# Kernel tuning notes

Measured on AMD Instinct MI355X. Metric: run time of the kernel, lower is better.

Reference implementation:

```python
import jax, jax.numpy as jnp
import numpy as np

WH, WW = 8, 8
N = WH * WW
DIM = 128
H = 4
B_ = 8192


def _make_buffers():
    # relative_coords_table: [1, 2Wh-1, 2Ww-1, 2]
    ch = np.arange(-(WH - 1), WH, dtype=np.float32)
    cw = np.arange(-(WW - 1), WW, dtype=np.float32)
    gh, gw = np.meshgrid(ch, cw, indexing='ij')
    table = np.stack([gh, gw], axis=-1)[None]  # [1, 2Wh-1, 2Ww-1, 2]
    table[..., 0] /= (WH - 1 + 1e-12)
    table[..., 1] /= (WW - 1 + 1e-12)
    table *= 8.0
    table = np.sign(table) * np.log2(np.abs(table) + 1.0) / np.log2(8.0)
    # relative_position_index: [N, N]
    yh, yw = np.meshgrid(np.arange(WH), np.arange(WW), indexing='ij')
    coords = np.stack([yh, yw]).reshape(2, -1)  # [2, N]
    rel = coords[:, :, None] - coords[:, None, :]  # [2, N, N]
    rel = rel.transpose(1, 2, 0).astype(np.int64)
    rel[..., 0] += WH - 1
    rel[..., 1] += WW - 1
    rel[..., 0] *= 2 * WW - 1
    idx = rel.sum(-1)
    return jnp.asarray(table, jnp.float32), jnp.asarray(idx, jnp.int32)


def setup_inputs() -> dict:
    key = jax.random.key(0)
    ks = jax.random.split(key, 9)
    s = 0.02
    rel_table, rel_index = _make_buffers()
    return {
        'x': jax.random.normal(ks[0], (B_, N, DIM), jnp.float32),
        'W_qkv': jax.random.normal(ks[1], (3 * DIM, DIM), jnp.float32) * s,
        'q_bias': jax.random.normal(ks[2], (DIM,), jnp.float32) * s,
        'v_bias': jax.random.normal(ks[3], (DIM,), jnp.float32) * s,
        'logit_scale': jnp.full((H, 1, 1), jnp.log(10.0), jnp.float32),
        'cpb_w1': jax.random.normal(ks[4], (512, 2), jnp.float32) * s,
        'cpb_b1': jax.random.normal(ks[5], (512,), jnp.float32) * s,
        'cpb_w2': jax.random.normal(ks[6], (H, 512), jnp.float32) * s,
        'proj_w': jax.random.normal(ks[7], (DIM, DIM), jnp.float32) * s,
        'proj_b': jax.random.normal(ks[8], (DIM,), jnp.float32) * s,
        'rel_table': rel_table,
        'rel_index': rel_index,
    }


def reference(x, W_qkv, q_bias, v_bias, logit_scale, cpb_w1, cpb_b1, cpb_w2,
              proj_w, proj_b, rel_table, rel_index):
    B, n, C = x.shape
    hd = C // H
    # qkv projection with Swin-V2 bias layout (k bias frozen at zero)
    qkv_bias = jnp.concatenate([q_bias, jnp.zeros_like(v_bias), v_bias])
    qkv = x @ W_qkv.T + qkv_bias               # [B, N, 3C]
    qkv = qkv.reshape(B, n, 3, H, hd).transpose(2, 0, 3, 1, 4)
    q, k, v = qkv[0], qkv[1], qkv[2]           # [B, H, N, hd]
    # cosine attention
    qn = q / jnp.maximum(jnp.linalg.norm(q, axis=-1, keepdims=True), 1e-12)
    kn = k / jnp.maximum(jnp.linalg.norm(k, axis=-1, keepdims=True), 1e-12)
    attn = jnp.einsum('bhnd,bhmd->bhnm', qn, kn)
    scale = jnp.exp(jnp.minimum(logit_scale, jnp.log(1.0 / 0.01)))  # [H,1,1]
    attn = attn * scale
    # continuous position bias MLP -> gather -> 16*sigmoid
    hmid = jax.nn.relu(rel_table @ cpb_w1.T + cpb_b1)      # [1,15,15,512]
    bias_table = (hmid @ cpb_w2.T).reshape(-1, H)          # [(2Wh-1)(2Ww-1), H]
    rpb = bias_table[rel_index.reshape(-1)].reshape(n, n, H)
    rpb = 16.0 * jax.nn.sigmoid(rpb.transpose(2, 0, 1))    # [H, N, N]
    attn = jax.nn.softmax(attn + rpb[None], axis=-1)
    out = jnp.einsum('bhnm,bhmd->bhnd', attn, v)           # [B, H, N, hd]
    out = out.transpose(0, 2, 1, 3).reshape(B, n, C)
    return out @ proj_w.T + proj_b
```

## Files before the change

kernel.cpp:

```cpp
#include <hip/hip_runtime.h>

typedef short bf16x8 __attribute__((ext_vector_type(8)));
typedef float f32x4 __attribute__((ext_vector_type(4)));

__device__ __forceinline__ unsigned cvt_pk_bf16(float lo, float hi) {
  unsigned r;
  asm("v_cvt_pk_bf16_f32 %0, %1, %2" : "=v"(r) : "v"(lo), "v"(hi));
  return r;
}

__device__ __forceinline__ bf16x8 pack4(unsigned a, unsigned b, unsigned c, unsigned d) {
  union { unsigned u[4]; bf16x8 v; } t;
  t.u[0] = a; t.u[1] = b; t.u[2] = c; t.u[3] = d;
  return t.v;
}

__device__ __forceinline__ unsigned short f2bf(float f) {
  unsigned u = __float_as_uint(f);
  unsigned r = (u + 0x7fffu + ((u >> 16) & 1u)) >> 16;
  return (unsigned short)r;
}

__global__ __launch_bounds__(256) void prep(
    const float* __restrict__ W_qkv, const float* __restrict__ proj_w,
    const float* __restrict__ cpb_w1, const float* __restrict__ cpb_b1,
    const float* __restrict__ cpb_w2, const float* __restrict__ rel_table,
    const int* __restrict__ rel_index,
    bf16x8* __restrict__ wq, bf16x8* __restrict__ wp, float* __restrict__ rpbf)
{
  const int b = blockIdx.x, t = threadIdx.x;
  if (b < 32) {
    int g = b * 256 + t;
    if (g < 6144) {
      int c = g >> 8, kk = (g >> 6) & 3, l = g & 63;
      const float* s = W_qkv + (c * 16 + (l & 15)) * 128 + kk * 32 + (l >> 4) * 8;
      bf16x8 v;
      #pragma unroll
      for (int j = 0; j < 8; ++j) v[j] = (short)f2bf(s[j]);
      wq[g] = v;
    } else {
      int gl = g - 6144;
      int c = gl >> 8, kk = (gl >> 6) & 3, l = gl & 63;
      const float* row = proj_w + (c * 16 + (l & 15)) * 128;
      bf16x8 v;
      #pragma unroll
      for (int j = 0; j < 8; ++j)
        v[j] = (short)f2bf(row[kk * 32 + (j >> 2) * 16 + (l >> 4) * 4 + (j & 3)]);
      wp[gl] = v;
    }
  } else {
    __shared__ float bt[900];
    if (t < 225) {
      float t0 = rel_table[t * 2], t1 = rel_table[t * 2 + 1];
      float a0 = 0.f, a1 = 0.f, a2 = 0.f, a3 = 0.f;
      for (int j = 0; j < 512; ++j) {
        float hm = fmaxf(t0 * cpb_w1[j * 2] + t1 * cpb_w1[j * 2 + 1] + cpb_b1[j], 0.f);
        a0 += hm * cpb_w2[j];
        a1 += hm * cpb_w2[512 + j];
        a2 += hm * cpb_w2[1024 + j];
        a3 += hm * cpb_w2[1536 + j];
      }
      bt[t * 4 + 0] = a0; bt[t * 4 + 1] = a1;
      bt[t * 4 + 2] = a2; bt[t * 4 + 3] = a3;
    }
    __syncthreads();
    for (int i = t; i < 16384; i += 256) {
      int hrc = i >> 8, lane = (i >> 2) & 63, j = i & 3;
      int hh = hrc >> 4, r = (hrc >> 2) & 3, c = hrc & 3;
      int n = r * 16 + (lane & 15);
      int m = c * 16 + ((lane >> 4) << 2) + j;
      float v = bt[rel_index[n * 64 + m] * 4 + hh];
      rpbf[i] = 16.0f * __fdividef(1.0f, 1.0f + __expf(-v));
    }
  }
}

__global__ __launch_bounds__(256, 3) void win_attn(
    const float* __restrict__ x,
    const float* __restrict__ q_bias,
    const float* __restrict__ v_bias,
    const float* __restrict__ logit_scale,
    const float* __restrict__ proj_b,
    const float* __restrict__ rpbf,
    const bf16x8* __restrict__ wq,
    const bf16x8* __restrict__ wp,
    float* __restrict__ out)
{
  __shared__ __align__(128) char lds[16384];
  const int tid  = threadIdx.x;
  const int lane = tid & 63;
  const int h    = tid >> 6;
  const int l15  = lane & 15;
  const int l4   = lane >> 4;
  const int swl  = (l15 & 7) << 4;
  const long base = (long)blockIdx.x * 8192;
  const f32x4 fzero = {0.f, 0.f, 0.f, 0.f};

  {
    const float4* xp = (const float4*)(x + base);
    #pragma unroll
    for (int i = 0; i < 8; ++i) {
      float4 v = xp[i * 256 + tid];
      int e   = (i * 256 + tid) * 4;
      int row = e >> 7;
      int cb  = (e & 127) * 2;
      uint2 pk = { cvt_pk_bf16(v.x, v.y), cvt_pk_bf16(v.z, v.w) };
      *(uint2*)(lds + ((row * 256 + cb) ^ ((row & 7) << 4))) = pk;
    }
  }
  __syncthreads();

  bf16x8 aq[4], bk[4], bv[2][2];

  {
    f32x4 qT[2][4], kT[2][4];
    #pragma unroll
    for (int ct = 0; ct < 2; ++ct)
      #pragma unroll
      for (int rt = 0; rt < 4; ++rt) { qT[ct][rt] = fzero; kT[ct][rt] = fzero; }

    #pragma unroll
    for (int kk = 0; kk < 4; ++kk) {
      bf16x8 a[4];
      #pragma unroll
      for (int rt = 0; rt < 4; ++rt) {
        int row = rt * 16 + l15;
        a[rt] = *(const bf16x8*)(lds + ((row * 256 + kk * 64 + l4 * 16) ^ swl));
      }
      #pragma unroll
      for (int ct = 0; ct < 2; ++ct) {
        bf16x8 wqf = wq[((2 * h + ct) * 4 + kk) * 64 + lane];
        bf16x8 wkf = wq[((8 + 2 * h + ct) * 4 + kk) * 64 + lane];
        #pragma unroll
        for (int rt = 0; rt < 4; ++rt) {
          qT[ct][rt] = __builtin_amdgcn_mfma_f32_16x16x32_bf16(wqf, a[rt], qT[ct][rt], 0, 0, 0);
          kT[ct][rt] = __builtin_amdgcn_mfma_f32_16x16x32_bf16(wkf, a[rt], kT[ct][rt], 0, 0, 0);
        }
      }
    }

    float scale = __expf(fminf(logit_scale[h], 4.6051701859880914f));
    float4 qb0 = *(const float4*)&q_bias[h * 32 + l4 * 4];
    float4 qb1 = *(const float4*)&q_bias[h * 32 + 16 + l4 * 4];
    #pragma unroll
    for (int rt = 0; rt < 4; ++rt) {
      float tq0 = qT[0][rt][0] + qb0.x, tq1 = qT[0][rt][1] + qb0.y;
      float tq2 = qT[0][rt][2] + qb0.z, tq3 = qT[0][rt][3] + qb0.w;
      float tq4 = qT[1][rt][0] + qb1.x, tq5 = qT[1][rt][1] + qb1.y;
      float tq6 = qT[1][rt][2] + qb1.z, tq7 = qT[1][rt][3] + qb1.w;
      float sq = tq0*tq0 + tq1*tq1 + tq2*tq2 + tq3*tq3
               + tq4*tq4 + tq5*tq5 + tq6*tq6 + tq7*tq7;
      float sk = kT[0][rt][0]*kT[0][rt][0] + kT[0][rt][1]*kT[0][rt][1]
               + kT[0][rt][2]*kT[0][rt][2] + kT[0][rt][3]*kT[0][rt][3]
               + kT[1][rt][0]*kT[1][rt][0] + kT[1][rt][1]*kT[1][rt][1]
               + kT[1][rt][2]*kT[1][rt][2] + kT[1][rt][3]*kT[1][rt][3];
      sq += __shfl_xor(sq, 16); sq += __shfl_xor(sq, 32);
      sk += __shfl_xor(sk, 16); sk += __shfl_xor(sk, 32);
      float iq = __fdividef(scale, fmaxf(sqrtf(sq), 1e-12f));
      float ik = __fdividef(1.0f,  fmaxf(sqrtf(sk), 1e-12f));
      aq[rt] = pack4(cvt_pk_bf16(tq0 * iq, tq1 * iq), cvt_pk_bf16(tq2 * iq, tq3 * iq),
                     cvt_pk_bf16(tq4 * iq, tq5 * iq), cvt_pk_bf16(tq6 * iq, tq7 * iq));
      bk[rt] = pack4(cvt_pk_bf16(kT[0][rt][0] * ik, kT[0][rt][1] * ik),
                     cvt_pk_bf16(kT[0][rt][2] * ik, kT[0][rt][3] * ik),
                     cvt_pk_bf16(kT[1][rt][0] * ik, kT[1][rt][1] * ik),
                     cvt_pk_bf16(kT[1][rt][2] * ik, kT[1][rt][3] * ik));
    }
  }

  {
    f32x4 vN[2][4];
    #pragma unroll
    for (int ct = 0; ct < 2; ++ct)
      #pragma unroll
      for (int rt = 0; rt < 4; ++rt) vN[ct][rt] = fzero;

    #pragma unroll
    for (int kk = 0; kk < 4; ++kk) {
      bf16x8 a[4];
      #pragma unroll
      for (int rt = 0; rt < 4; ++rt) {
        int row = rt * 16 + l15;
        a[rt] = *(const bf16x8*)(lds + ((row * 256 + kk * 64 + l4 * 16) ^ swl));
      }
      #pragma unroll
      for (int ct = 0; ct < 2; ++ct) {
        bf16x8 wvf = wq[((16 + 2 * h + ct) * 4 + kk) * 64 + lane];
        #pragma unroll
        for (int rt = 0; rt < 4; ++rt)
          vN[ct][rt] = __builtin_amdgcn_mfma_f32_16x16x32_bf16(a[rt], wvf, vN[ct][rt], 0, 0, 0);
      }
    }
    __syncthreads();

    float vb0 = v_bias[h * 32 + l15], vb1 = v_bias[h * 32 + 16 + l15];
    #pragma unroll
    for (int ks = 0; ks < 2; ++ks)
      #pragma unroll
      for (int ct = 0; ct < 2; ++ct) {
        float vb = ct ? vb1 : vb0;
        bv[ks][ct] = pack4(
            cvt_pk_bf16(vN[ct][2 * ks][0] + vb, vN[ct][2 * ks][1] + vb),
            cvt_pk_bf16(vN[ct][2 * ks][2] + vb, vN[ct][2 * ks][3] + vb),
            cvt_pk_bf16(vN[ct][2 * ks + 1][0] + vb, vN[ct][2 * ks + 1][1] + vb),
            cvt_pk_bf16(vN[ct][2 * ks + 1][2] + vb, vN[ct][2 * ks + 1][3] + vb));
      }
  }

  {
    const f32x4* rp = (const f32x4*)rpbf;
    #pragma unroll
    for (int r = 0; r < 4; ++r) {
      f32x4 st[4];
      #pragma unroll
      for (int c = 0; c < 4; ++c)
        st[c] = __builtin_amdgcn_mfma_f32_16x16x32_bf16(
            bk[c], aq[r], rp[(h * 16 + r * 4 + c) * 64 + lane], 0, 0, 0);

      float mx = st[0][0];
      #pragma unroll
      for (int c = 0; c < 4; ++c)
        #pragma unroll
        for (int j = 0; j < 4; ++j) mx = fmaxf(mx, st[c][j]);
      mx = fmaxf(mx, __shfl_xor(mx, 16));
      mx = fmaxf(mx, __shfl_xor(mx, 32));

      float e[4][4];
      float sum = 0.f;
      #pragma unroll
      for (int c = 0; c < 4; ++c)
        #pragma unroll
        for (int j = 0; j < 4; ++j) { e[c][j] = __expf(st[c][j] - mx); sum += e[c][j]; }
      sum += __shfl_xor(sum, 16); sum += __shfl_xor(sum, 32);
      float rs = __fdividef(1.0f, sum);

      bf16x8 ap0 = pack4(cvt_pk_bf16(e[0][0], e[0][1]), cvt_pk_bf16(e[0][2], e[0][3]),
                         cvt_pk_bf16(e[1][0], e[1][1]), cvt_pk_bf16(e[1][2], e[1][3]));
      bf16x8 ap1 = pack4(cvt_pk_bf16(e[2][0], e[2][1]), cvt_pk_bf16(e[2][2], e[2][3]),
                         cvt_pk_bf16(e[3][0], e[3][1]), cvt_pk_bf16(e[3][2], e[3][3]));

      f32x4 o0 = __builtin_amdgcn_mfma_f32_16x16x32_bf16(bv[0][0], ap0, fzero, 0, 0, 0);
      o0 = __builtin_amdgcn_mfma_f32_16x16x32_bf16(bv[1][0], ap1, o0, 0, 0, 0);
      f32x4 o1 = __builtin_amdgcn_mfma_f32_16x16x32_bf16(bv[0][1], ap0, fzero, 0, 0, 0);
      o1 = __builtin_amdgcn_mfma_f32_16x16x32_bf16(bv[1][1], ap1, o1, 0, 0, 0);

      int n = r * 16 + l15;
      uint4 w = { cvt_pk_bf16(o0[0] * rs, o0[1] * rs), cvt_pk_bf16(o0[2] * rs, o0[3] * rs),
                  cvt_pk_bf16(o1[0] * rs, o1[1] * rs), cvt_pk_bf16(o1[2] * rs, o1[3] * rs) };
      *(uint4*)(lds + ((n * 256 + h * 64 + 16 * l4) ^ ((n & 7) << 4))) = w;
    }
  }
  __syncthreads();

  {
    const int n = h * 16 + l15;
    f32x4 po[8];
    #pragma unroll
    for (int c2 = 0; c2 < 8; ++c2) po[c2] = fzero;
    #pragma unroll
    for (int kk = 0; kk < 4; ++kk) {
      bf16x8 ob = *(const bf16x8*)(lds + ((n * 256 + kk * 64 + 16 * l4) ^ swl));
      #pragma unroll
      for (int c2 = 0; c2 < 8; ++c2) {
        bf16x8 wf = wp[(c2 * 4 + kk) * 64 + lane];
        po[c2] = __builtin_amdgcn_mfma_f32_16x16x32_bf16(wf, ob, po[c2], 0, 0, 0);
      }
    }
    float* op = out + base + (long)n * 128;
    #pragma unroll
    for (int c2 = 0; c2 < 8; ++c2) {
      float4 pb = *(const float4*)&proj_b[c2 * 16 + l4 * 4];
      f32x4 v = { po[c2][0] + pb.x, po[c2][1] + pb.y,
                  po[c2][2] + pb.z, po[c2][3] + pb.w };
      __builtin_nontemporal_store(v, (f32x4*)&op[c2 * 16 + l4 * 4]);
    }
  }
}

extern "C" void kernel_launch(void* const* d_in, const int* in_sizes, int n_in,
                              void* d_out, int out_size, void* d_ws, size_t ws_size,
                              hipStream_t stream) {
  (void)n_in; (void)out_size; (void)ws_size;
  const float* x           = (const float*)d_in[0];
  const float* W_qkv       = (const float*)d_in[1];
  const float* q_bias      = (const float*)d_in[2];
  const float* v_bias      = (const float*)d_in[3];
  const float* logit_scale = (const float*)d_in[4];
  const float* cpb_w1      = (const float*)d_in[5];
  const float* cpb_b1      = (const float*)d_in[6];
  const float* cpb_w2      = (const float*)d_in[7];
  const float* proj_w      = (const float*)d_in[8];
  const float* proj_b      = (const float*)d_in[9];
  const float* rel_table   = (const float*)d_in[10];
  const int*   rel_index   = (const int*)d_in[11];

  float*  rpbf = (float*)d_ws;
  bf16x8* wq   = (bf16x8*)((char*)d_ws + 65536);
  bf16x8* wp   = (bf16x8*)((char*)d_ws + 65536 + 98304);

  int nwin = in_sizes[0] / 8192;

  prep<<<33, 256, 0, stream>>>(W_qkv, proj_w, cpb_w1, cpb_b1, cpb_w2,
                               rel_table, rel_index, wq, wp, rpbf);
  win_attn<<<nwin, 256, 0, stream>>>(x, q_bias, v_bias, logit_scale, proj_b,
                                     rpbf, wq, wp, (float*)d_out);
}
```

Before: 221.1 us.

## Use exp2 softmax with prescaled logits, add MFMA priority hints, repartition projection

Folds log2(e) into the cosine-attention scale and the position-bias table (16*log2e), so the softmax can use exp2f directly. Wraps MFMA blocks in s_setprio raises so matrix work is favoured over other waves. Changes the output projection so each wave computes all 64 rows for its own two 16-column tiles instead of 16 rows by all 128 columns. The weight fragments loaded per wave drop to a quarter, at the cost of four LDS reads per kk step, and the non-temporal stores become ordinary stores.

New measurement: 250.9 us. 13.5% more time.

```diff
diff --git a/kernel.cpp b/kernel.cpp
--- a/kernel.cpp
+++ b/kernel.cpp
@@ -70,7 +70,7 @@
       int n = r * 16 + (lane & 15);
       int m = c * 16 + ((lane >> 4) << 2) + j;
       float v = bt[rel_index[n * 64 + m] * 4 + hh];
-      rpbf[i] = 16.0f * __fdividef(1.0f, 1.0f + __expf(-v));
+      rpbf[i] = 23.083120654223414f * __fdividef(1.0f, 1.0f + __expf(-v));
     }
   }
 }
@@ -131,15 +131,18 @@
       for (int ct = 0; ct < 2; ++ct) {
         bf16x8 wqf = wq[((2 * h + ct) * 4 + kk) * 64 + lane];
         bf16x8 wkf = wq[((8 + 2 * h + ct) * 4 + kk) * 64 + lane];
+        __builtin_amdgcn_s_setprio(1);
         #pragma unroll
         for (int rt = 0; rt < 4; ++rt) {
           qT[ct][rt] = __builtin_amdgcn_mfma_f32_16x16x32_bf16(wqf, a[rt], qT[ct][rt], 0, 0, 0);
           kT[ct][rt] = __builtin_amdgcn_mfma_f32_16x16x32_bf16(wkf, a[rt], kT[ct][rt], 0, 0, 0);
         }
-      }
-    }
-
-    float scale = __expf(fminf(logit_scale[h], 4.6051701859880914f));
+        __builtin_amdgcn_s_setprio(0);
+      }
+    }
+
+    float scale = __expf(fminf(logit_scale[h], 4.6051701859880914f))
+                * 1.4426950408889634f;
     float4 qb0 = *(const float4*)&q_bias[h * 32 + l4 * 4];
     float4 qb1 = *(const float4*)&q_bias[h * 32 + 16 + l4 * 4];
     #pragma unroll
@@ -185,9 +188,11 @@
       #pragma unroll
       for (int ct = 0; ct < 2; ++ct) {
         bf16x8 wvf = wq[((16 + 2 * h + ct) * 4 + kk) * 64 + lane];
+        __builtin_amdgcn_s_setprio(1);
         #pragma unroll
         for (int rt = 0; rt < 4; ++rt)
           vN[ct][rt] = __builtin_amdgcn_mfma_f32_16x16x32_bf16(a[rt], wvf, vN[ct][rt], 0, 0, 0);
+        __builtin_amdgcn_s_setprio(0);
       }
     }
     __syncthreads();
@@ -211,10 +216,12 @@
     #pragma unroll
     for (int r = 0; r < 4; ++r) {
       f32x4 st[4];
+      __builtin_amdgcn_s_setprio(1);
       #pragma unroll
       for (int c = 0; c < 4; ++c)
         st[c] = __builtin_amdgcn_mfma_f32_16x16x32_bf16(
             bk[c], aq[r], rp[(h * 16 + r * 4 + c) * 64 + lane], 0, 0, 0);
+      __builtin_amdgcn_s_setprio(0);
 
       float mx = st[0][0];
       #pragma unroll
@@ -229,7 +236,7 @@
       #pragma unroll
       for (int c = 0; c < 4; ++c)
         #pragma unroll
-        for (int j = 0; j < 4; ++j) { e[c][j] = __expf(st[c][j] - mx); sum += e[c][j]; }
+        for (int j = 0; j < 4; ++j) { e[c][j] = exp2f(st[c][j] - mx); sum += e[c][j]; }
       sum += __shfl_xor(sum, 16); sum += __shfl_xor(sum, 32);
       float rs = __fdividef(1.0f, sum);
 
@@ -238,10 +245,12 @@
       bf16x8 ap1 = pack4(cvt_pk_bf16(e[2][0], e[2][1]), cvt_pk_bf16(e[2][2], e[2][3]),
                          cvt_pk_bf16(e[3][0], e[3][1]), cvt_pk_bf16(e[3][2], e[3][3]));
 
+      __builtin_amdgcn_s_setprio(1);
       f32x4 o0 = __builtin_amdgcn_mfma_f32_16x16x32_bf16(bv[0][0], ap0, fzero, 0, 0, 0);
       o0 = __builtin_amdgcn_mfma_f32_16x16x32_bf16(bv[1][0], ap1, o0, 0, 0, 0);
       f32x4 o1 = __builtin_amdgcn_mfma_f32_16x16x32_bf16(bv[0][1], ap0, fzero, 0, 0, 0);
       o1 = __builtin_amdgcn_mfma_f32_16x16x32_bf16(bv[1][1], ap1, o1, 0, 0, 0);
+      __builtin_amdgcn_s_setprio(0);
 
       int n = r * 16 + l15;
       uint4 w = { cvt_pk_bf16(o0[0] * rs, o0[1] * rs), cvt_pk_bf16(o0[2] * rs, o0[3] * rs),
@@ -252,26 +261,42 @@
   __syncthreads();
 
   {
-    const int n = h * 16 + l15;
-    f32x4 po[8];
-    #pragma unroll
-    for (int c2 = 0; c2 < 8; ++c2) po[c2] = fzero;
+    f32x4 po[4][2];
+    #pragma unroll
+    for (int rt = 0; rt < 4; ++rt)
+      #pragma unroll
+      for (int ci = 0; ci < 2; ++ci) po[rt][ci] = fzero;
+
     #pragma unroll
     for (int kk = 0; kk < 4; ++kk) {
-      bf16x8 ob = *(const bf16x8*)(lds + ((n * 256 + kk * 64 + 16 * l4) ^ swl));
-      #pragma unroll
-      for (int c2 = 0; c2 < 8; ++c2) {
-        bf16x8 wf = wp[(c2 * 4 + kk) * 64 + lane];
-        po[c2] = __builtin_amdgcn_mfma_f32_16x16x32_bf16(wf, ob, po[c2], 0, 0, 0);
-      }
-    }
-    float* op = out + base + (long)n * 128;
-    #pragma unroll
-    for (int c2 = 0; c2 < 8; ++c2) {
+      bf16x8 ob[4];
+      #pragma unroll
+      for (int rt = 0; rt < 4; ++rt) {
+        int row = rt * 16 + l15;
+        ob[rt] = *(const bf16x8*)(lds + ((row * 256 + kk * 64 + 16 * l4) ^ swl));
+      }
+      #pragma unroll
+      for (int ci = 0; ci < 2; ++ci) {
+        bf16x8 wf = wp[((2 * h + ci) * 4 + kk) * 64 + lane];
+        __builtin_amdgcn_s_setprio(1);
+        #pragma unroll
+        for (int rt = 0; rt < 4; ++rt)
+          po[rt][ci] = __builtin_amdgcn_mfma_f32_16x16x32_bf16(wf, ob[rt], po[rt][ci], 0, 0, 0);
+        __builtin_amdgcn_s_setprio(0);
+      }
+    }
+
+    #pragma unroll
+    for (int ci = 0; ci < 2; ++ci) {
+      int c2 = 2 * h + ci;
       float4 pb = *(const float4*)&proj_b[c2 * 16 + l4 * 4];
-      f32x4 v = { po[c2][0] + pb.x, po[c2][1] + pb.y,
-                  po[c2][2] + pb.z, po[c2][3] + pb.w };
-      __builtin_nontemporal_store(v, (f32x4*)&op[c2 * 16 + l4 * 4]);
+      #pragma unroll
+      for (int rt = 0; rt < 4; ++rt) {
+        float* op = out + base + (long)(rt * 16 + l15) * 128 + c2 * 16 + l4 * 4;
+        float4 v = { po[rt][ci][0] + pb.x, po[rt][ci][1] + pb.y,
+                     po[rt][ci][2] + pb.z, po[rt][ci][3] + pb.w };
+        *(float4*)op = v;
+      }
     }
   }
 }
```
